# Kernel tuning notes

Measured on AMD Instinct MI355X. Metric: run time of the kernel, lower is better.

Reference implementation:

```python
import jax, jax.numpy as jnp
import numpy as np

B, T, C, H, D = 4, 2048, 1024, 16, 64
EPS = 1e-5

def setup_inputs() -> dict:
    key = jax.random.key(0)
    ks = jax.random.split(key, 8)
    s = lambda fan_in: 1.0 / np.sqrt(fan_in)
    return {
        'x': jax.random.normal(ks[0], (B, T, C), jnp.float32),
        'wq': jax.random.normal(ks[1], (H, C, D), jnp.float32) * s(C),
        'wk': jax.random.normal(ks[2], (H, C, D), jnp.float32) * s(C),
        'wv': jax.random.normal(ks[3], (H, C, D), jnp.float32) * s(C),
        'w_proj': jax.random.normal(ks[4], (C, C), jnp.float32) * s(C),
        'b_proj': jnp.zeros((C,), jnp.float32),
        'w1': jax.random.normal(ks[5], (C, 4 * C), jnp.float32) * s(C),
        'b1': jnp.zeros((4 * C,), jnp.float32),
        'w2': jax.random.normal(ks[6], (4 * C, C), jnp.float32) * s(4 * C),
        'b2': jnp.zeros((C,), jnp.float32),
        'g1': jnp.ones((C,), jnp.float32),
        'be1': jnp.zeros((C,), jnp.float32),
        'g2': jnp.ones((C,), jnp.float32),
        'be2': jnp.zeros((C,), jnp.float32),
    }

def layer_norm(x, g, b):
    mu = jnp.mean(x, axis=-1, keepdims=True)
    var = jnp.mean(jnp.square(x - mu), axis=-1, keepdims=True)
    return (x - mu) * jax.lax.rsqrt(var + EPS) * g + b

def reference(x, wq, wk, wv, w_proj, b_proj, w1, b1, w2, b2, g1, be1, g2, be2):
    # --- attention (pre-LN) ---
    xn = layer_norm(x, g1, be1)
    q = jnp.einsum('btc,hcd->bhtd', xn, wq)
    k = jnp.einsum('btc,hcd->bhtd', xn, wk)
    v = jnp.einsum('btc,hcd->bhtd', xn, wv)
    # NOTE: original scales by full embedding dim C (not head size)
    scores = jnp.einsum('bhtd,bhsd->bhts', q, k) * (C ** -0.5)
    causal = jnp.tril(jnp.ones((T, T), bool))
    scores = jnp.where(causal, scores, -jnp.inf)
    wei = jax.nn.softmax(scores, axis=-1)
    attn = jnp.einsum('bhts,bhsd->bhtd', wei, v)
    attn = attn.transpose(0, 2, 1, 3).reshape(B, T, C)  # concat heads
    x = x + attn @ w_proj + b_proj
    # --- FFN (pre-LN) ---
    xn2 = layer_norm(x, g2, be2)
    h = jax.nn.relu(xn2 @ w1 + b1)
    x = x + h @ w2 + b2
    return x
```

## Files before the change

kernel.cpp:

```cpp
#include <hip/hip_runtime.h>
#include <hip/hip_bf16.h>

#define B_ 4
#define T_ 2048
#define C_ 1024
#define H_ 16
#define D_ 64
#define M_ (B_*T_)

typedef unsigned short ushort;
typedef __attribute__((ext_vector_type(8))) short short8;
typedef __attribute__((ext_vector_type(8))) unsigned short ushort8;
typedef __attribute__((ext_vector_type(4))) float floatx4;
typedef __attribute__((ext_vector_type(4))) unsigned int uintx4;

static __device__ __forceinline__ float bf2f(ushort u) {
    unsigned int x = ((unsigned int)u) << 16;
    return __builtin_bit_cast(float, x);
}
static __device__ __forceinline__ ushort f2bf(float f) {
    unsigned int x = __builtin_bit_cast(unsigned int, f);
    unsigned int r = (x + 0x7fffu + ((x >> 16) & 1u)) >> 16;
    return (ushort)r;
}

typedef const __attribute__((address_space(1))) unsigned int gu32;
typedef __attribute__((address_space(3))) unsigned int lu32;
static __device__ __forceinline__ void glds16(const void* g, void* l) {
    __builtin_amdgcn_global_load_lds((gu32*)g, (lu32*)l, 16, 0, 0);
}

__global__ __launch_bounds__(256) void ln_kernel(
    const float* __restrict__ x, const float* __restrict__ g,
    const float* __restrict__ be, ushort* __restrict__ out)
{
    int row = blockIdx.x;
    int tid = threadIdx.x;
    const float* xr = x + (size_t)row * C_;
    float v[4];
    float s = 0.f, s2 = 0.f;
#pragma unroll
    for (int i = 0; i < 4; i++) {
        float t = xr[tid + i * 256];
        v[i] = t; s += t; s2 += t * t;
    }
#pragma unroll
    for (int off = 32; off; off >>= 1) {
        s  += __shfl_down(s, off);
        s2 += __shfl_down(s2, off);
    }
    __shared__ float rs[4], rs2[4];
    __shared__ float smu, srstd;
    int w = tid >> 6;
    if ((tid & 63) == 0) { rs[w] = s; rs2[w] = s2; }
    __syncthreads();
    if (tid == 0) {
        float ts  = rs[0] + rs[1] + rs[2] + rs[3];
        float ts2 = rs2[0] + rs2[1] + rs2[2] + rs2[3];
        float mu  = ts * (1.f / C_);
        float var = ts2 * (1.f / C_) - mu * mu;
        smu = mu; srstd = rsqrtf(var + 1e-5f);
    }
    __syncthreads();
    float mu = smu, r = srstd;
#pragma unroll
    for (int i = 0; i < 4; i++) {
        int c = tid + i * 256;
        out[(size_t)row * C_ + c] = f2bf((v[i] - mu) * r * g[c] + be[c]);
    }
}

__global__ __launch_bounds__(256) void transpose_conv(
    const float* __restrict__ in, ushort* __restrict__ out,
    int R, int Cn, long long in_bstride, long long out_bstride)
{
    __shared__ float tile[32][33];
    const float* ip = in + (size_t)blockIdx.z * in_bstride;
    ushort* op = out + (size_t)blockIdx.z * out_bstride;
    int tx = threadIdx.x;
    int ty = threadIdx.y;
    int c0 = blockIdx.x * 32, r0 = blockIdx.y * 32;
#pragma unroll
    for (int i = 0; i < 32; i += 8) {
        tile[ty + i][tx] = ip[(size_t)(r0 + ty + i) * Cn + c0 + tx];
    }
    __syncthreads();
#pragma unroll
    for (int i = 0; i < 32; i += 8) {
        int oc = c0 + ty + i;
        int orr = r0 + tx;
        op[(size_t)oc * R + orr] = f2bf(tile[tx][ty + i]);
    }
}

__global__ __launch_bounds__(256) void vtrans_kernel(
    const ushort* __restrict__ qkv, ushort* __restrict__ VtG)
{
    int bh = blockIdx.y;
    int b = bh >> 4, h = bh & 15;
    int j0 = blockIdx.x * 64;
    int tid = threadIdx.x;
    __shared__ unsigned int X[64 * 33];
    const ushort* Vg = qkv + (size_t)(b * T_) * 3072 + 2048 + h * 64;
#pragma unroll
    for (int it = 0; it < 2; it++) {
        int j = (tid >> 3) + it * 32;
        int dp = (tid & 7) * 4;
        uintx4 val = *(const uintx4*)(Vg + (size_t)(j0 + j) * 3072 + dp * 2);
#pragma unroll
        for (int k = 0; k < 4; k++) X[j * 33 + dp + k] = val[k];
    }
    __syncthreads();
    int dp = tid >> 3, jc = tid & 7;
    unsigned int v[8];
#pragma unroll
    for (int jj = 0; jj < 8; jj++) v[jj] = X[(jc * 8 + jj) * 33 + dp];
    ushort8 lo, hi;
#pragma unroll
    for (int jj = 0; jj < 8; jj++) {
        lo[jj] = (ushort)(v[jj] & 0xffffu);
        hi[jj] = (ushort)(v[jj] >> 16);
    }
    size_t r0 = ((size_t)(h * 256 + 4 * (2 * dp) + b)) * T_ + j0 + jc * 8;
    size_t r1 = ((size_t)(h * 256 + 4 * (2 * dp + 1) + b)) * T_ + j0 + jc * 8;
    *(ushort8*)&VtG[r0] = lo;
    *(ushort8*)&VtG[r1] = hi;
}

template<bool OUTBF16, bool BIAS, bool RELU, bool RESID>
__global__ __launch_bounds__(256, 2) void gemm_kernel(
    const ushort* __restrict__ A,
    const ushort* __restrict__ Bt,
    const float* __restrict__ bias,
    const float* __restrict__ resid,
    void* __restrict__ Cout,
    int Ndim, int K, int Nt)
{
    __shared__ ushort As[2][128 * 64];
    __shared__ ushort Bs[2][128 * 64];
    int bid = blockIdx.x;
    int xcd = bid & 7;
    int loc = bid >> 3;
    int m0 = (xcd * 8 + loc / Nt) * 128;
    int n0 = (loc % Nt) * 128;

    int tid = threadIdx.x;
    int wave = tid >> 6, lane = tid & 63;
    int quad = lane >> 4, l16 = lane & 15;
    int wm = (wave >> 1) * 64, wn = (wave & 1) * 64;
    floatx4 acc[4][4] = {};

    int lrow = lane >> 3;
    int lchunk = (lane & 7) ^ (lrow & 7);
    const ushort* Ab = A  + (size_t)m0 * K + lchunk * 8;
    const ushort* Bb = Bt + (size_t)n0 * K + lchunk * 8;

    int nK = K >> 6;
#pragma unroll
    for (int it = 0; it < 4; it++) {
        int rb = wave * 32 + it * 8;
        int r  = rb + lrow;
        glds16(Ab + (size_t)r * K, &As[0][rb * 64]);
        glds16(Bb + (size_t)r * K, &Bs[0][rb * 64]);
    }

    for (int ki = 0; ki < nK; ki++) {
        int buf = ki & 1;
        __syncthreads();
        if (ki + 1 < nK) {
            int kn = (ki + 1) * 64;
#pragma unroll
            for (int it = 0; it < 4; it++) {
                int rb = wave * 32 + it * 8;
                int r  = rb + lrow;
                glds16(Ab + (size_t)r * K + kn, &As[buf ^ 1][rb * 64]);
                glds16(Bb + (size_t)r * K + kn, &Bs[buf ^ 1][rb * 64]);
            }
        }
#pragma unroll
        for (int kk = 0; kk < 2; kk++) {
            short8 af[4], bfv[4];
            int c = kk * 4 + quad;
            int sw = (c ^ (l16 & 7)) * 8;
#pragma unroll
            for (int mi = 0; mi < 4; mi++)
                af[mi] = *(const short8*)&As[buf][(wm + mi * 16 + l16) * 64 + sw];
#pragma unroll
            for (int ni = 0; ni < 4; ni++)
                bfv[ni] = *(const short8*)&Bs[buf][(wn + ni * 16 + l16) * 64 + sw];
#pragma unroll
            for (int mi = 0; mi < 4; mi++)
#pragma unroll
                for (int ni = 0; ni < 4; ni++)
                    acc[mi][ni] = __builtin_amdgcn_mfma_f32_16x16x32_bf16(af[mi], bfv[ni], acc[mi][ni], 0, 0, 0);
        }
    }

    int r4 = quad * 4;
#pragma unroll
    for (int mi = 0; mi < 4; mi++) {
#pragma unroll
        for (int ni = 0; ni < 4; ni++) {
#pragma unroll
            for (int r = 0; r < 4; r++) {
                int gm = m0 + wm + mi * 16 + r4 + r;
                int gn = n0 + wn + ni * 16 + l16;
                float v = acc[mi][ni][r];
                if (BIAS)  v += bias[gn];
                if (RESID) v += resid[(size_t)gm * Ndim + gn];
                if (RELU)  v = fmaxf(v, 0.f);
                if (OUTBF16) ((ushort*)Cout)[(size_t)gm * Ndim + gn] = f2bf(v);
                else         ((float*)Cout)[(size_t)gm * Ndim + gn] = v;
            }
        }
    }
}

__global__ __launch_bounds__(256, 2) void attn_kernel(
    const ushort* __restrict__ qkv,
    const ushort* __restrict__ VtG,
    ushort* __restrict__ attnb)
{
    const int LD = 3072;
    int bid = blockIdx.x;
    int bh = (bid & 7) * 8 + ((bid >> 3) & 7);
    int qt = 15 - (bid >> 6);
    int b = bh >> 4, h = bh & 15;
    int t0 = qt * 128;
    int tid = threadIdx.x;
    int wave = tid >> 6, lane = tid & 63;
    int quad = lane >> 4, l16 = lane & 15;

    __shared__ ushort Ks[2][64 * 64];
    __shared__ ushort Vt[2][64 * 64];
    __shared__ ushort Ps[4][32 * 72];

    const ushort* Qg = qkv + (size_t)(b * T_) * LD + h * 64;
    const ushort* Kg = Qg + 1024;
    const ushort* VtB = VtG + (size_t)(h * 256 + b) * T_;

    int qrow_base = t0 + wave * 32;
    int lrow = lane >> 3;
    int lchunk = (lane & 7) ^ (lrow & 7);

    short8 qa[2][2];
#pragma unroll
    for (int mt = 0; mt < 2; mt++) {
        const ushort* qp = Qg + (size_t)(qrow_base + mt * 16 + l16) * LD + quad * 8;
        ushort8 q0 = *(const ushort8*)qp;
        ushort8 q1 = *(const ushort8*)(qp + 32);
        ushort8 a0, a1;
#pragma unroll
        for (int d = 0; d < 8; d++) {
            a0[d] = f2bf(bf2f(q0[d]) * 0.03125f);
            a1[d] = f2bf(bf2f(q1[d]) * 0.03125f);
        }
        qa[mt][0] = __builtin_bit_cast(short8, a0);
        qa[mt][1] = __builtin_bit_cast(short8, a1);
    }

    float l_part[2][4];
    floatx4 o_acc[2][4];
#pragma unroll
    for (int mt = 0; mt < 2; mt++)
#pragma unroll
        for (int r = 0; r < 4; r++) {
            l_part[mt][r] = 0.f;
            o_acc[mt][r] = floatx4{0.f, 0.f, 0.f, 0.f};
        }

    int nIter = t0 / 64 + 2;

#pragma unroll
    for (int it = 0; it < 2; it++) {
        int rb = (wave * 2 + it) * 8;
        int r = rb + lrow;
        glds16(Kg  + (size_t)r * LD + lchunk * 8, &Ks[0][rb * 64]);
        glds16(VtB + (size_t)r * (4 * T_) + lchunk * 8, &Vt[0][rb * 64]);
    }

    for (int ii = 0; ii < nIter; ii++) {
        int s0 = ii * 64;
        int buf = ii & 1;
        __syncthreads();
        if (ii + 1 < nIter) {
            int sn = s0 + 64;
#pragma unroll
            for (int it = 0; it < 2; it++) {
                int rb = (wave * 2 + it) * 8;
                int r = rb + lrow;
                glds16(Kg  + (size_t)(sn + r) * LD + lchunk * 8, &Ks[buf ^ 1][rb * 64]);
                glds16(VtB + (size_t)r * (4 * T_) + sn + lchunk * 8, &Vt[buf ^ 1][rb * 64]);
            }
        }

        if (s0 <= qrow_base + 31) {
#pragma unroll
            for (int mt = 0; mt < 2; mt++) {
                floatx4 s_acc[4];
#pragma unroll
                for (int nt = 0; nt < 4; nt++) {
                    int krow = nt * 16 + l16;
                    const short8* kb0 = (const short8*)&Ks[buf][krow * 64 + ((quad       ^ (l16 & 7)) * 8)];
                    const short8* kb1 = (const short8*)&Ks[buf][krow * 64 + (((4 + quad) ^ (l16 & 7)) * 8)];
                    floatx4 z = {0.f, 0.f, 0.f, 0.f};
                    z = __builtin_amdgcn_mfma_f32_16x16x32_bf16(qa[mt][0], *kb0, z, 0, 0, 0);
                    s_acc[nt] = __builtin_amdgcn_mfma_f32_16x16x32_bf16(qa[mt][1], *kb1, z, 0, 0, 0);
                }
                int base_mt = qrow_base + mt * 16;
                if (s0 + 63 > base_mt) {
#pragma unroll
                    for (int nt = 0; nt < 4; nt++)
#pragma unroll
                        for (int r = 0; r < 4; r++) {
                            int gi = base_mt + quad * 4 + r;
                            int gj = s0 + nt * 16 + l16;
                            if (gj > gi) s_acc[nt][r] = -INFINITY;
                        }
                }
#pragma unroll
                for (int nt = 0; nt < 4; nt++)
#pragma unroll
                    for (int r = 0; r < 4; r++) {
                        float e = __expf(s_acc[nt][r]);
                        s_acc[nt][r] = e;
                        l_part[mt][r] += e;
                        Ps[wave][(mt * 16 + quad * 4 + r) * 72 + nt * 16 + l16] = f2bf(e);
                    }
            }
            asm volatile("s_waitcnt lgkmcnt(0)" ::: "memory");
            short8 pa[2][2];
#pragma unroll
            for (int mt = 0; mt < 2; mt++) {
                pa[mt][0] = *(const short8*)&Ps[wave][(mt * 16 + l16) * 72 + quad * 8];
                pa[mt][1] = *(const short8*)&Ps[wave][(mt * 16 + l16) * 72 + quad * 8 + 32];
            }
#pragma unroll
            for (int dt = 0; dt < 4; dt++) {
                int vrow = dt * 16 + l16;
                const short8* vb0 = (const short8*)&Vt[buf][vrow * 64 + ((quad       ^ (l16 & 7)) * 8)];
                const short8* vb1 = (const short8*)&Vt[buf][vrow * 64 + (((4 + quad) ^ (l16 & 7)) * 8)];
#pragma unroll
                for (int mt = 0; mt < 2; mt++) {
                    o_acc[mt][dt] = __builtin_amdgcn_mfma_f32_16x16x32_bf16(pa[mt][0], *vb0, o_acc[mt][dt], 0, 0, 0);
                    o_acc[mt][dt] = __builtin_amdgcn_mfma_f32_16x16x32_bf16(pa[mt][1], *vb1, o_acc[mt][dt], 0, 0, 0);
                }
            }
        }
    }

#pragma unroll
    for (int mt = 0; mt < 2; mt++)
#pragma unroll
        for (int r = 0; r < 4; r++) {
            float ls = l_part[mt][r];
            ls += __shfl_xor(ls, 1);
            ls += __shfl_xor(ls, 2);
            ls += __shfl_xor(ls, 4);
            ls += __shfl_xor(ls, 8);
            float inv = 1.f / ls;
            int gi = qrow_base + mt * 16 + quad * 4 + r;
            ushort* op = attnb + (size_t)(b * T_ + gi) * 1024 + h * 64;
#pragma unroll
            for (int dt = 0; dt < 4; dt++)
                op[dt * 16 + l16] = f2bf(o_acc[mt][dt][r] * inv);
        }
}

extern "C" void kernel_launch(void* const* d_in, const int* in_sizes, int n_in,
                              void* d_out, int out_size, void* d_ws, size_t ws_size,
                              hipStream_t stream) {
    (void)in_sizes; (void)n_in; (void)out_size; (void)ws_size;
    const float* x      = (const float*)d_in[0];
    const float* wq     = (const float*)d_in[1];
    const float* wk     = (const float*)d_in[2];
    const float* wv     = (const float*)d_in[3];
    const float* w_proj = (const float*)d_in[4];
    const float* b_proj = (const float*)d_in[5];
    const float* w1     = (const float*)d_in[6];
    const float* b1     = (const float*)d_in[7];
    const float* w2     = (const float*)d_in[8];
    const float* b2     = (const float*)d_in[9];
    const float* g1     = (const float*)d_in[10];
    const float* be1    = (const float*)d_in[11];
    const float* g2     = (const float*)d_in[12];
    const float* be2    = (const float*)d_in[13];
    float* out = (float*)d_out;

    char* ws = (char*)d_ws;
    const size_t MB = 1024ull * 1024ull;
    ushort* xn     = (ushort*)(ws + 0);
    ushort* qkv    = (ushort*)(ws + 16 * MB);
    ushort* attnb  = (ushort*)(ws + 64 * MB);
    ushort* hbuf   = (ushort*)(ws + 16 * MB);
    float*  x1     = (float*) (ws + 80 * MB);
    ushort* VtG    = (ushort*)(ws + 80 * MB);
    ushort* WqkvT  = (ushort*)(ws + 112 * MB);
    ushort* WprojT = (ushort*)(ws + 118 * MB);
    ushort* W1T    = (ushort*)(ws + 120 * MB);
    ushort* W2T    = (ushort*)(ws + 128 * MB);
    ushort* xn2 = xn;

    dim3 tb(32, 8);
    ln_kernel<<<M_, 256, 0, stream>>>(x, g1, be1, xn);
    transpose_conv<<<dim3(D_ / 32, C_ / 32, H_), tb, 0, stream>>>(wq, WqkvT,               C_, D_, (long long)C_ * D_, (long long)D_ * C_);
    transpose_conv<<<dim3(D_ / 32, C_ / 32, H_), tb, 0, stream>>>(wk, WqkvT + C_ * C_,     C_, D_, (long long)C_ * D_, (long long)D_ * C_);
    transpose_conv<<<dim3(D_ / 32, C_ / 32, H_), tb, 0, stream>>>(wv, WqkvT + 2 * C_ * C_, C_, D_, (long long)C_ * D_, (long long)D_ * C_);
    transpose_conv<<<dim3(C_ / 32, C_ / 32, 1), tb, 0, stream>>>(w_proj, WprojT, C_, C_, 0, 0);
    transpose_conv<<<dim3(4 * C_ / 32, C_ / 32, 1), tb, 0, stream>>>(w1, W1T, C_, 4 * C_, 0, 0);
    transpose_conv<<<dim3(C_ / 32, 4 * C_ / 32, 1), tb, 0, stream>>>(w2, W2T, 4 * C_, C_, 0, 0);
    gemm_kernel<true, false, false, false><<<64 * 24, 256, 0, stream>>>(
        xn, WqkvT, nullptr, nullptr, qkv, 3072, C_, 24);
    vtrans_kernel<<<dim3(T_ / 64, B_ * H_), 256, 0, stream>>>(qkv, VtG);
    attn_kernel<<<1024, 256, 0, stream>>>(qkv, VtG, attnb);
    gemm_kernel<false, true, false, true><<<64 * 8, 256, 0, stream>>>(
        attnb, WprojT, b_proj, x, x1, C_, C_, 8);
    ln_kernel<<<M_, 256, 0, stream>>>(x1, g2, be2, xn2);
    gemm_kernel<true, true, true, false><<<64 * 32, 256, 0, stream>>>(
        xn2, W1T, b1, nullptr, hbuf, 4 * C_, C_, 32);
    gemm_kernel<false, true, false, true><<<64 * 8, 256, 0, stream>>>(
        hbuf, W2T, b2, x1, out, C_, 4 * C_, 8);
}
```

Measured before the change: 471.0 us.

## Fuse weight transposes into one launch and add single-buffer GEMM variant

Merges the six weight transpose/convert launches into one kernel that dispatches on block index. Adds a template flag so the K=1024 GEMMs (QKV and W1) use a single LDS buffer with a load-sync-compute loop, halving shared memory to allow more resident blocks. The K=4096 and projection GEMMs keep double buffering. It also changes the block-to-tile mapping so consecutive blocks on one XCD share an n-tile instead of an m-tile. Single buffering gives up the overlap between global loads and MFMA compute.

```diff
diff --git a/kernel.cpp b/kernel.cpp
--- a/kernel.cpp
+++ b/kernel.cpp
@@ -70,26 +70,52 @@
     }
 }
 
-__global__ __launch_bounds__(256) void transpose_conv(
+static __device__ __forceinline__ void do_transpose(
     const float* __restrict__ in, ushort* __restrict__ out,
-    int R, int Cn, long long in_bstride, long long out_bstride)
+    int R, int Cn, int bx, int by)
 {
     __shared__ float tile[32][33];
-    const float* ip = in + (size_t)blockIdx.z * in_bstride;
-    ushort* op = out + (size_t)blockIdx.z * out_bstride;
     int tx = threadIdx.x;
     int ty = threadIdx.y;
-    int c0 = blockIdx.x * 32, r0 = blockIdx.y * 32;
+    int c0 = bx * 32, r0 = by * 32;
 #pragma unroll
     for (int i = 0; i < 32; i += 8) {
-        tile[ty + i][tx] = ip[(size_t)(r0 + ty + i) * Cn + c0 + tx];
+        tile[ty + i][tx] = in[(size_t)(r0 + ty + i) * Cn + c0 + tx];
     }
     __syncthreads();
 #pragma unroll
     for (int i = 0; i < 32; i += 8) {
         int oc = c0 + ty + i;
         int orr = r0 + tx;
-        op[(size_t)oc * R + orr] = f2bf(tile[tx][ty + i]);
+        out[(size_t)oc * R + orr] = f2bf(tile[tx][ty + i]);
+    }
+}
+
+__global__ __launch_bounds__(256) void wt_fused_kernel(
+    const float* __restrict__ wq, const float* __restrict__ wk, const float* __restrict__ wv,
+    const float* __restrict__ w_proj, const float* __restrict__ w1, const float* __restrict__ w2,
+    ushort* __restrict__ WqkvT, ushort* __restrict__ WprojT,
+    ushort* __restrict__ W1T, ushort* __restrict__ W2T)
+{
+    int id = blockIdx.x;
+    if (id < 3072) {
+        int which = id >> 10;
+        int lid = id & 1023;
+        int bz = lid >> 6;
+        int rem = lid & 63;
+        int by = rem >> 1, bx = rem & 1;
+        const float* in = (which == 0 ? wq : which == 1 ? wk : wv) + (size_t)bz * C_ * D_;
+        ushort* out = WqkvT + (size_t)which * C_ * C_ + (size_t)bz * D_ * C_;
+        do_transpose(in, out, C_, D_, bx, by);
+    } else if (id < 4096) {
+        int lid = id - 3072;
+        do_transpose(w_proj, WprojT, C_, C_, lid & 31, lid >> 5);
+    } else if (id < 8192) {
+        int lid = id - 4096;
+        do_transpose(w1, W1T, C_, 4 * C_, lid & 127, lid >> 7);
+    } else {
+        int lid = id - 8192;
+        do_transpose(w2, W2T, 4 * C_, C_, lid & 31, lid >> 5);
     }
 }
 
@@ -127,7 +153,7 @@
     *(ushort8*)&VtG[r1] = hi;
 }
 
-template<bool OUTBF16, bool BIAS, bool RELU, bool RESID>
+template<bool OUTBF16, bool BIAS, bool RELU, bool RESID, bool DBUF>
 __global__ __launch_bounds__(256, 2) void gemm_kernel(
     const ushort* __restrict__ A,
     const ushort* __restrict__ Bt,
@@ -136,13 +162,14 @@
     void* __restrict__ Cout,
     int Ndim, int K, int Nt)
 {
-    __shared__ ushort As[2][128 * 64];
-    __shared__ ushort Bs[2][128 * 64];
+    constexpr int NB = DBUF ? 2 : 1;
+    __shared__ ushort As[NB][128 * 64];
+    __shared__ ushort Bs[NB][128 * 64];
     int bid = blockIdx.x;
     int xcd = bid & 7;
     int loc = bid >> 3;
-    int m0 = (xcd * 8 + loc / Nt) * 128;
-    int n0 = (loc % Nt) * 128;
+    int m0 = (xcd * 8 + (loc & 7)) * 128;
+    int n0 = (loc >> 3) * 128;
 
     int tid = threadIdx.x;
     int wave = tid >> 6, lane = tid & 63;
@@ -156,26 +183,40 @@
     const ushort* Bb = Bt + (size_t)n0 * K + lchunk * 8;
 
     int nK = K >> 6;
-#pragma unroll
-    for (int it = 0; it < 4; it++) {
-        int rb = wave * 32 + it * 8;
-        int r  = rb + lrow;
-        glds16(Ab + (size_t)r * K, &As[0][rb * 64]);
-        glds16(Bb + (size_t)r * K, &Bs[0][rb * 64]);
+    if (DBUF) {
+#pragma unroll
+        for (int it = 0; it < 4; it++) {
+            int rb = wave * 32 + it * 8;
+            int r  = rb + lrow;
+            glds16(Ab + (size_t)r * K, &As[0][rb * 64]);
+            glds16(Bb + (size_t)r * K, &Bs[0][rb * 64]);
+        }
     }
 
     for (int ki = 0; ki < nK; ki++) {
-        int buf = ki & 1;
+        int buf = DBUF ? (ki & 1) : 0;
         __syncthreads();
-        if (ki + 1 < nK) {
-            int kn = (ki + 1) * 64;
+        if (DBUF) {
+            if (ki + 1 < nK) {
+                int kn = (ki + 1) * 64;
+#pragma unroll
+                for (int it = 0; it < 4; it++) {
+                    int rb = wave * 32 + it * 8;
+                    int r  = rb + lrow;
+                    glds16(Ab + (size_t)r * K + kn, &As[buf ^ 1][rb * 64]);
+                    glds16(Bb + (size_t)r * K + kn, &Bs[buf ^ 1][rb * 64]);
+                }
+            }
+        } else {
+            int kn = ki * 64;
 #pragma unroll
             for (int it = 0; it < 4; it++) {
                 int rb = wave * 32 + it * 8;
                 int r  = rb + lrow;
-                glds16(Ab + (size_t)r * K + kn, &As[buf ^ 1][rb * 64]);
-                glds16(Bb + (size_t)r * K + kn, &Bs[buf ^ 1][rb * 64]);
-            }
+                glds16(Ab + (size_t)r * K + kn, &As[0][rb * 64]);
+                glds16(Bb + (size_t)r * K + kn, &Bs[0][rb * 64]);
+            }
+            __syncthreads();
         }
 #pragma unroll
         for (int kk = 0; kk < 2; kk++) {
@@ -401,23 +442,18 @@
     ushort* W2T    = (ushort*)(ws + 128 * MB);
     ushort* xn2 = xn;
 
-    dim3 tb(32, 8);
     ln_kernel<<<M_, 256, 0, stream>>>(x, g1, be1, xn);
-    transpose_conv<<<dim3(D_ / 32, C_ / 32, H_), tb, 0, stream>>>(wq, WqkvT,               C_, D_, (long long)C_ * D_, (long long)D_ * C_);
-    transpose_conv<<<dim3(D_ / 32, C_ / 32, H_), tb, 0, stream>>>(wk, WqkvT + C_ * C_,     C_, D_, (long long)C_ * D_, (long long)D_ * C_);
-    transpose_conv<<<dim3(D_ / 32, C_ / 32, H_), tb, 0, stream>>>(wv, WqkvT + 2 * C_ * C_, C_, D_, (long long)C_ * D_, (long long)D_ * C_);
-    transpose_conv<<<dim3(C_ / 32, C_ / 32, 1), tb, 0, stream>>>(w_proj, WprojT, C_, C_, 0, 0);
-    transpose_conv<<<dim3(4 * C_ / 32, C_ / 32, 1), tb, 0, stream>>>(w1, W1T, C_, 4 * C_, 0, 0);
-    transpose_conv<<<dim3(C_ / 32, 4 * C_ / 32, 1), tb, 0, stream>>>(w2, W2T, 4 * C_, C_, 0, 0);
-    gemm_kernel<true, false, false, false><<<64 * 24, 256, 0, stream>>>(
+    wt_fused_kernel<<<12288, dim3(32, 8), 0, stream>>>(
+        wq, wk, wv, w_proj, w1, w2, WqkvT, WprojT, W1T, W2T);
+    gemm_kernel<true, false, false, false, false><<<64 * 24, 256, 0, stream>>>(
         xn, WqkvT, nullptr, nullptr, qkv, 3072, C_, 24);
     vtrans_kernel<<<dim3(T_ / 64, B_ * H_), 256, 0, stream>>>(qkv, VtG);
     attn_kernel<<<1024, 256, 0, stream>>>(qkv, VtG, attnb);
-    gemm_kernel<false, true, false, true><<<64 * 8, 256, 0, stream>>>(
+    gemm_kernel<false, true, false, true, true><<<64 * 8, 256, 0, stream>>>(
         attnb, WprojT, b_proj, x, x1, C_, C_, 8);
     ln_kernel<<<M_, 256, 0, stream>>>(x1, g2, be2, xn2);
-    gemm_kernel<true, true, true, false><<<64 * 32, 256, 0, stream>>>(
+    gemm_kernel<true, true, true, false, false><<<64 * 32, 256, 0, stream>>>(
         xn2, W1T, b1, nullptr, hbuf, 4 * C_, C_, 32);
-    gemm_kernel<false, true, false, true><<<64 * 8, 256, 0, stream>>>(
+    gemm_kernel<false, true, false, true, true><<<64 * 8, 256, 0, stream>>>(
         hbuf, W2T, b2, x1, out, C_, 4 * C_, 8);
 }
```

Result: no change. 465.8 us (-1.1%).
